# Kernel optimization log

Hardware: AMD Instinct MI355X
Metric: run time of the kernel (lower is better)

## Reference

```python
import math
import jax, jax.numpy as jnp
import numpy as np

N_HEAD = 8
EPS = 1e-4

def _ln(x, g, b):
    m = jnp.mean(x, axis=-1, keepdims=True)
    v = jnp.mean((x - m) ** 2, axis=-1, keepdims=True)
    return (x - m) * jax.lax.rsqrt(v + EPS) * g + b

def _rel_bias(T, rel_w):
    # rel_pos_mat[i,j] = j - i, shifted to [0, 2T-2]; one-hot @ W == table lookup
    pos = jnp.arange(T)
    idx = pos[None, :] - pos[:, None] + (T - 1)        # [T,T]
    return rel_w[idx].transpose(2, 0, 1)               # [n_head,T,T]

def _attn(x, qw, qb, kw, kb, vw, vb, pw, pb, rel_pos):
    B, T, C = x.shape
    hd = C // N_HEAD
    q = (x @ qw + qb).reshape(B, T, N_HEAD, hd)
    k = (x @ kw + kb).reshape(B, T, N_HEAD, hd)
    v = (x @ vw + vb).reshape(B, T, N_HEAD, hd)
    att = jnp.einsum('bqhd,bkhd->bhqk', q, k) * (1.0 / math.sqrt(hd))
    att = att + rel_pos[None]
    att = jax.nn.softmax(att, axis=-1)
    y = jnp.einsum('bhqk,bkhd->bqhd', att, v).reshape(B, T, C)
    return y @ pw + pb

def setup_inputs() -> dict:
    key = jax.random.key(0)
    C, H, W, B = 512, 64, 64, 8
    ks = iter(jax.random.split(key, 40))
    d = {}
    d['x'] = jax.random.normal(next(ks), (B, H * W, C), jnp.float32)
    def w(shape):
        return jax.random.normal(next(ks), shape, jnp.float32) * 0.02
    for p in ('row', 'col'):
        for nm in ('q', 'k', 'v', 'p'):
            d[f'{p}_{nm}w'] = w((C, C))
            d[f'{p}_{nm}b'] = jnp.zeros((C,), jnp.float32)
    for nm in ('rln1', 'cln1', 'ln2'):
        d[f'{nm}_g'] = jnp.ones((C,), jnp.float32)
        d[f'{nm}_b'] = jnp.zeros((C,), jnp.float32)
    d['ff_w1'] = w((C, 4 * C)); d['ff_b1'] = jnp.zeros((4 * C,), jnp.float32)
    d['ff_w2'] = w((4 * C, C)); d['ff_b2'] = jnp.zeros((C,), jnp.float32)
    d['row_rel_w'] = w((2 * H - 1, N_HEAD))
    d['col_rel_w'] = w((2 * W - 1, N_HEAD))
    return d

def reference(x,
              row_qw, row_qb, row_kw, row_kb, row_vw, row_vb, row_pw, row_pb,
              col_qw, col_qb, col_kw, col_kb, col_vw, col_vb, col_pw, col_pb,
              rln1_g, rln1_b, cln1_g, cln1_b, ln2_g, ln2_b,
              ff_w1, ff_b1, ff_w2, ff_b2, row_rel_w, col_rel_w):
    b, n, c = x.shape
    h = w = int(math.isqrt(n))
    # row attention: over h within each column -> batch b*w
    xr = x.reshape(b, h, w, c).transpose(0, 2, 1, 3).reshape(b * w, h, c)
    x_row = _attn(_ln(xr, rln1_g, rln1_b),
                  row_qw, row_qb, row_kw, row_kb, row_vw, row_vb, row_pw, row_pb,
                  _rel_bias(h, row_rel_w))
    x_row = x_row.reshape(b, w, h, c).transpose(0, 2, 1, 3).reshape(b, h * w, c)
    # col attention: over w within each row -> batch b*h
    xc = xr.reshape(b, w, h, c).transpose(0, 2, 1, 3).reshape(b * h, w, c)
    x_col = _attn(_ln(xc, cln1_g, cln1_b),
                  col_qw, col_qb, col_kw, col_kb, col_vw, col_vb, col_pw, col_pb,
                  _rel_bias(w, col_rel_w))
    x_col = x_col.reshape(b, h * w, c)
    out = x + x_row + x_col
    hdd = _ln(out, ln2_g, ln2_b) @ ff_w1 + ff_b1
    hdd = jax.nn.gelu(hdd, approximate=False)
    out = out + (hdd @ ff_w2 + ff_b2)
    return out
```

## Files before the change

kernel.cpp:

```cpp
#include <hip/hip_runtime.h>

typedef unsigned short u16;
typedef unsigned int   u32;
typedef float  f32x4  __attribute__((ext_vector_type(4)));
typedef u32    u32x4  __attribute__((ext_vector_type(4)));
typedef __bf16 bf16x8 __attribute__((ext_vector_type(8)));

#define DEV __device__ __forceinline__

DEV float b2f(u16 u){ return __uint_as_float(((u32)u) << 16); }
DEV u16 f2b(float f){
  u32 u = __float_as_uint(f);
  u32 r = 0x7FFFu + ((u >> 16) & 1u);
  return (u16)((u + r) >> 16);
}
DEV u32 pack2(float a, float b){ return (u32)f2b(a) | ((u32)f2b(b) << 16); }
DEV uint4 pack8(const float* o){
  uint4 r;
  r.x = pack2(o[0], o[1]); r.y = pack2(o[2], o[3]);
  r.z = pack2(o[4], o[5]); r.w = pack2(o[6], o[7]);
  return r;
}

DEV f32x4 mfma16(u32x4 a, u32x4 b, f32x4 c){
  return __builtin_amdgcn_mfma_f32_16x16x32_bf16(
      __builtin_bit_cast(bf16x8, a), __builtin_bit_cast(bf16x8, b), c, 0, 0, 0);
}

DEV void gload16(const u16* g, u16* l){
  __builtin_amdgcn_global_load_lds((const __attribute__((address_space(1))) void*)(g),
                                   (__attribute__((address_space(3))) void*)(l), 16, 0, 0);
}

__global__ __launch_bounds__(256) void tranb3(
    const float* __restrict__ sA, const float* __restrict__ sB,
    const float* __restrict__ sC,
    u16* __restrict__ dA, u16* __restrict__ dB, u16* __restrict__ dC){
  __shared__ float tile[32][33];
  const float* src = (blockIdx.z == 0) ? sA : (blockIdx.z == 1) ? sB : sC;
  u16* dst = (blockIdx.z == 0) ? dA : (blockIdx.z == 1) ? dB : dC;
  const int bx = blockIdx.x * 32, by = blockIdx.y * 32;
  const int tx = threadIdx.x, ty = threadIdx.y;
#pragma unroll
  for (int i = 0; i < 4; ++i)
    tile[ty + i * 8][tx] = src[(size_t)(by + ty + i * 8) * 512 + bx + tx];
  __syncthreads();
#pragma unroll
  for (int i = 0; i < 4; ++i)
    dst[(size_t)(bx + ty + i * 8) * 512 + by + tx] = f2b(tile[tx][ty + i * 8]);
}

__global__ __launch_bounds__(256) void tranbP(const float* __restrict__ src,
                                              u16* __restrict__ dst, int off){
  __shared__ float tile[32][33];
  const int bx = blockIdx.x * 32, by = blockIdx.y * 32;
  const int tx = threadIdx.x, ty = threadIdx.y;
#pragma unroll
  for (int i = 0; i < 4; ++i)
    tile[ty + i * 8][tx] = src[(size_t)(by + ty + i * 8) * 512 + bx + tx];
  __syncthreads();
#pragma unroll
  for (int i = 0; i < 4; ++i)
    dst[(size_t)(bx + ty + i * 8) * 1024 + off + by + tx] = f2b(tile[tx][ty + i * 8]);
}

__global__ __launch_bounds__(256) void tranb(const float* __restrict__ src, u16* __restrict__ dst,
                                             int R, int C){
  __shared__ float tile[32][33];
  const int bx = blockIdx.x * 32, by = blockIdx.y * 32;
  const int tx = threadIdx.x, ty = threadIdx.y;
#pragma unroll
  for (int i = 0; i < 4; ++i)
    tile[ty + i * 8][tx] = src[(size_t)(by + ty + i * 8) * C + bx + tx];
  __syncthreads();
#pragma unroll
  for (int i = 0; i < 4; ++i)
    dst[(size_t)(bx + ty + i * 8) * R + by + tx] = f2b(tile[tx][ty + i * 8]);
}

template<int TWO>
__global__ __launch_bounds__(256) void ln_k(const float* __restrict__ x,
    const float* __restrict__ g1, const float* __restrict__ b1,
    const float* __restrict__ g2, const float* __restrict__ b2,
    u16* __restrict__ y1, u16* __restrict__ y2){
  const int tid = threadIdx.x, lane = tid & 63, wv = tid >> 6;
  const size_t row  = (size_t)blockIdx.x * 4 + wv;
  const size_t boff = row * 512 + lane * 8;
  float f[8];
  {
    const f32x4* p = (const f32x4*)(x + boff);
    const f32x4 a = p[0], b = p[1];
#pragma unroll
    for (int j = 0; j < 4; ++j){ f[j] = a[j]; f[4 + j] = b[j]; }
  }
  float s1 = 0.f, s2 = 0.f;
#pragma unroll
  for (int j = 0; j < 8; ++j){ s1 += f[j]; s2 += f[j] * f[j]; }
#pragma unroll
  for (int off = 32; off > 0; off >>= 1){
    s1 += __shfl_xor(s1, off);
    s2 += __shfl_xor(s2, off);
  }
  const float m   = s1 * (1.0f / 512.0f);
  const float var = s2 * (1.0f / 512.0f) - m * m;
  const float inv = rsqrtf(var + 1e-4f);
  const int cb = lane * 8;
  float o[8];
#pragma unroll
  for (int j = 0; j < 8; ++j) o[j] = (f[j] - m) * inv * g1[cb + j] + b1[cb + j];
  *(uint4*)(y1 + boff) = pack8(o);
  if (TWO){
#pragma unroll
    for (int j = 0; j < 8; ++j) o[j] = (f[j] - m) * inv * g2[cb + j] + b2[cb + j];
    *(uint4*)(y2 + boff) = pack8(o);
  }
}

template<int EPI, bool FUSE3>
__global__ __launch_bounds__(512, 4) void gemmW(const u16* __restrict__ A,
    const u16* __restrict__ A2nd, int nkA,
    const u16* __restrict__ Bt, int ldb,
    const float* __restrict__ b0p, const float* __restrict__ b1p,
    const float* __restrict__ b2p,
    const float* __restrict__ res,
    void* __restrict__ out0, void* __restrict__ out1, void* __restrict__ out2,
    int Nd, int K, int lda){
  __shared__ __align__(16) u16 smem[32768];
  const int tid  = threadIdx.x;
  const int lane = tid & 63;
  const int lr = lane & 15, lg = lane >> 4;
  const int wave = tid >> 6;
  const int wm = (wave >> 2) * 64, wn = (wave & 3) * 64;
  const u32 fd  = blockIdx.y * gridDim.x + blockIdx.x;
  const u32 cpx = (gridDim.x * gridDim.y) >> 3;
  const u32 T   = (fd & 7) * cpx + (fd >> 3);
  const int m0 = (T / gridDim.x) * 128, n0 = (T % gridDim.x) * 256;
  const int nk = K >> 5;

  f32x4 acc[4][4] = {};

  auto stage = [&](int buf, int kt){
    const u16* Ap; int kb;
    if (kt < nkA){ Ap = A;    kb = kt * 32; }
    else         { Ap = A2nd; kb = (kt - nkA) * 32; }
    const int kbB = kt * 32;
    const int ao = buf * 12288, bo = ao + 4096;
    {
      const int r = tid >> 2, gc = (tid & 3) ^ ((r >> 1) & 3);
      gload16(Ap + (size_t)(m0 + r) * lda + kb + gc * 8, smem + ao + tid * 8);
    }
#pragma unroll
    for (int i = 0; i < 2; ++i){
      const int c = i * 512 + tid;
      const int r = c >> 2, gc = (c & 3) ^ ((r >> 1) & 3);
      gload16(Bt + (size_t)(n0 + r) * ldb + kbB + gc * 8, smem + bo + c * 8);
    }
  };

  stage(0, 0);
  int cur = 0;
  for (int kt = 0; kt < nk; ++kt){
    if (kt + 1 < nk){
      stage(cur ^ 1, kt + 1);
      asm volatile("s_waitcnt vmcnt(3)" ::: "memory");
    } else {
      asm volatile("s_waitcnt vmcnt(0)" ::: "memory");
    }
    __builtin_amdgcn_s_barrier();
    __builtin_amdgcn_sched_barrier(0);
    const int ao = cur * 12288, bo = ao + 4096;
    u32x4 af[4], bf[4];
#pragma unroll
    for (int mt = 0; mt < 4; ++mt){
      const int row = wm + mt * 16 + lr;
      const int js = lg ^ ((row >> 1) & 3);
      af[mt] = *(const u32x4*)&smem[ao + row * 32 + js * 8];
    }
#pragma unroll
    for (int nt = 0; nt < 4; ++nt){
      const int row = wn + nt * 16 + lr;
      const int js = lg ^ ((row >> 1) & 3);
      bf[nt] = *(const u32x4*)&smem[bo + row * 32 + js * 8];
    }
    __builtin_amdgcn_s_setprio(1);
#pragma unroll
    for (int mt = 0; mt < 4; ++mt)
#pragma unroll
      for (int nt = 0; nt < 4; ++nt)
        acc[mt][nt] = mfma16(af[mt], bf[nt], acc[mt][nt]);
    __builtin_amdgcn_s_setprio(0);
    asm volatile("" ::: "memory");
    __builtin_amdgcn_sched_barrier(0);
    __builtin_amdgcn_s_barrier();
    cur ^= 1;
  }

  if (EPI == 2){
    float* Cf = (float*)smem;
    float* o = (float*)out0;
#pragma unroll
    for (int h = 0; h < 2; ++h){
      if ((wave >> 2) == h){
#pragma unroll
        for (int mt = 0; mt < 4; ++mt)
#pragma unroll
          for (int nt = 0; nt < 4; ++nt){
            const int col = wn + nt * 16 + lr;
            float bv = b0p ? b0p[n0 + col] : 0.0f;
            if (b1p) bv += b1p[n0 + col];
#pragma unroll
            for (int r = 0; r < 4; ++r)
              Cf[(mt * 16 + lg * 4 + r) * 256 + col] = acc[mt][nt][r] + bv;
          }
      }
      __syncthreads();
#pragma unroll
      for (int p = 0; p < 8; ++p){
        const int rr = p * 8 + (tid >> 6);
        const int cc = (tid & 63) * 4;
        f32x4 c = *(f32x4*)&Cf[rr * 256 + cc];
        const size_t gi = (size_t)(m0 + h * 64 + rr) * Nd + n0 + cc;
        c += *(const f32x4*)(res + gi);
        *(f32x4*)(o + gi) = c;
      }
      __syncthreads();
    }
  } else {
    u16* Cl = smem;
#pragma unroll
    for (int mt = 0; mt < 4; ++mt)
#pragma unroll
      for (int nt = 0; nt < 4; ++nt){
        const int col = n0 + wn + nt * 16 + lr;
        float bv;
        if (FUSE3){
          if (col >= 1024)      bv = b2p[col - 1024];
          else if (col >= 512)  bv = b1p[col - 512];
          else                  bv = b0p[col];
        } else bv = b0p[col];
#pragma unroll
        for (int r = 0; r < 4; ++r){
          float v2 = acc[mt][nt][r] + bv;
          if (EPI == 1) v2 = 0.5f * v2 * (1.0f + erff(v2 * 0.70710678118654752f));
          Cl[(wm + mt * 16 + lg * 4 + r) * 256 + wn + nt * 16 + lr] = f2b(v2);
        }
      }
    __syncthreads();
    u16* o = (u16*)out0;
    int ncol = n0;
    if (FUSE3){
      const int grp = n0 >> 9;
      o = (u16*)(grp == 0 ? out0 : grp == 1 ? out1 : out2);
      ncol = n0 & 511;
    }
#pragma unroll
    for (int p = 0; p < 8; ++p){
      const int rr = p * 16 + (tid >> 5);
      const int cc = (tid & 31) * 8;
      *(uint4*)(o + (size_t)(m0 + rr) * (FUSE3 ? 512 : Nd) + ncol + cc) =
          *(uint4*)&Cl[rr * 256 + cc];
    }
  }
}

__global__ __launch_bounds__(256, 2) void attn64(u16* __restrict__ q,
    const u16* __restrict__ k, const u16* __restrict__ v,
    const float* __restrict__ relw,
    int sscale, int tstr){
  __shared__ __align__(16) u16 Qs[64 * 80];
  __shared__ __align__(16) u16 Ks[64 * 80];
  __shared__ __align__(16) u16 Vt[64 * 80];
  __shared__ __align__(16) u16 Ps[64 * 80];
  __shared__ float Ss[64 * 68];
  __shared__ float tb[128];

  const int s = blockIdx.x, head = blockIdx.y;
  const int tid = threadIdx.x;
  const int lane = tid & 63, wv = tid >> 6;
  const int lr = lane & 15, lg = lane >> 4;
  const int base = (s >> 6) * 4096 + (s & 63) * sscale;

  if (tid < 127) tb[tid] = relw[tid * 8 + head];

#pragma unroll
  for (int rep = 0; rep < 2; ++rep){
    const int e = rep * 2048 + tid * 8;
    const int t = e >> 6, c = e & 63;
    const size_t goff = (size_t)(base + t * tstr) * 512 + head * 64 + c;
    *(uint4*)&Qs[t * 80 + c] = *(const uint4*)(q + goff);
    *(uint4*)&Ks[t * 80 + c] = *(const uint4*)(k + goff);
    const uint4 vvv = *(const uint4*)(v + goff);
    u32 w;
    w = vvv.x; Vt[(c + 0) * 80 + t] = (u16)w; Vt[(c + 1) * 80 + t] = (u16)(w >> 16);
    w = vvv.y; Vt[(c + 2) * 80 + t] = (u16)w; Vt[(c + 3) * 80 + t] = (u16)(w >> 16);
    w = vvv.z; Vt[(c + 4) * 80 + t] = (u16)w; Vt[(c + 5) * 80 + t] = (u16)(w >> 16);
    w = vvv.w; Vt[(c + 6) * 80 + t] = (u16)w; Vt[(c + 7) * 80 + t] = (u16)(w >> 16);
  }
  __syncthreads();

  const int i0 = wv * 16;
  u32x4 af[2];
#pragma unroll
  for (int kk = 0; kk < 2; ++kk)
    af[kk] = *(const u32x4*)&Qs[(i0 + lr) * 80 + kk * 32 + lg * 8];
#pragma unroll
  for (int jt = 0; jt < 4; ++jt){
    f32x4 acc = {};
#pragma unroll
    for (int kk = 0; kk < 2; ++kk){
      const u32x4 bf = *(const u32x4*)&Ks[(jt * 16 + lr) * 80 + kk * 32 + lg * 8];
      acc = mfma16(af[kk], bf, acc);
    }
#pragma unroll
    for (int r = 0; r < 4; ++r){
      const int i = i0 + lg * 4 + r;
      const int j = jt * 16 + lr;
      Ss[i * 68 + j] = acc[r] * 0.125f + tb[j - i + 63];
    }
  }
  __syncthreads();

  {
    const int rr = tid >> 2, cp = tid & 3;
    float ev[16];
    float mx = -3.0e38f;
#pragma unroll
    for (int u = 0; u < 16; ++u){ ev[u] = Ss[rr * 68 + cp * 16 + u]; mx = fmaxf(mx, ev[u]); }
    mx = fmaxf(mx, __shfl_xor(mx, 1, 4));
    mx = fmaxf(mx, __shfl_xor(mx, 2, 4));
    float sum = 0.f;
#pragma unroll
    for (int u = 0; u < 16; ++u){ ev[u] = expf(ev[u] - mx); sum += ev[u]; }
    sum += __shfl_xor(sum, 1, 4);
    sum += __shfl_xor(sum, 2, 4);
    const float inv = 1.0f / sum;
#pragma unroll
    for (int u = 0; u < 16; ++u) Ps[rr * 80 + cp * 16 + u] = f2b(ev[u] * inv);
  }
  __syncthreads();

  u32x4 pa[2];
#pragma unroll
  for (int kk = 0; kk < 2; ++kk)
    pa[kk] = *(const u32x4*)&Ps[(i0 + lr) * 80 + kk * 32 + lg * 8];
#pragma unroll
  for (int dt = 0; dt < 4; ++dt){
    f32x4 acc = {};
#pragma unroll
    for (int kk = 0; kk < 2; ++kk){
      const u32x4 bf = *(const u32x4*)&Vt[(dt * 16 + lr) * 80 + kk * 32 + lg * 8];
      acc = mfma16(pa[kk], bf, acc);
    }
#pragma unroll
    for (int r = 0; r < 4; ++r)
      Qs[(i0 + lg * 4 + r) * 80 + dt * 16 + lr] = f2b(acc[r]);
  }
  __syncthreads();

#pragma unroll
  for (int p = 0; p < 2; ++p){
    const int rr = p * 32 + (tid >> 3);
    const int cc = (tid & 7) * 8;
    *(uint4*)(q + (size_t)(base + rr * tstr) * 512 + head * 64 + cc) =
        *(uint4*)&Qs[rr * 80 + cc];
  }
}

extern "C" void kernel_launch(void* const* d_in, const int* in_sizes, int n_in,
                              void* d_out, int out_size, void* d_ws, size_t ws_size,
                              hipStream_t stream){
  const float* x      = (const float*)d_in[0];
  const float* row_qw = (const float*)d_in[1];  const float* row_qb = (const float*)d_in[2];
  const float* row_kw = (const float*)d_in[3];  const float* row_kb = (const float*)d_in[4];
  const float* row_vw = (const float*)d_in[5];  const float* row_vb = (const float*)d_in[6];
  const float* row_pw = (const float*)d_in[7];  const float* row_pb = (const float*)d_in[8];
  const float* col_qw = (const float*)d_in[9];  const float* col_qb = (const float*)d_in[10];
  const float* col_kw = (const float*)d_in[11]; const float* col_kb = (const float*)d_in[12];
  const float* col_vw = (const float*)d_in[13]; const float* col_vb = (const float*)d_in[14];
  const float* col_pw = (const float*)d_in[15]; const float* col_pb = (const float*)d_in[16];
  const float* rg  = (const float*)d_in[17]; const float* rb  = (const float*)d_in[18];
  const float* cg  = (const float*)d_in[19]; const float* cb  = (const float*)d_in[20];
  const float* l2g = (const float*)d_in[21]; const float* l2b = (const float*)d_in[22];
  const float* ffw1 = (const float*)d_in[23]; const float* ffb1 = (const float*)d_in[24];
  const float* ffw2 = (const float*)d_in[25]; const float* ffb2 = (const float*)d_in[26];
  const float* rrel = (const float*)d_in[27]; const float* crel = (const float*)d_in[28];
  float* outp = (float*)d_out;
  u16* outp16 = (u16*)d_out;

  const size_t ACT = (size_t)32768 * 512;
  const size_t W55 = (size_t)512 * 512;
  const size_t NEED = (4 * ACT + 8 * W55) * 2;
  if (ws_size < NEED) return;

  u16* A0 = (u16*)d_ws;
  u16* A1 = A0 + ACT;
  u16* A2 = A1 + ACT;
  u16* A3 = A2 + ACT;
  u16* D0 = outp16;
  u16* D1 = outp16 + ACT;
  u16* wtb = A3 + ACT;
  u16* wt_q = wtb;  u16* wt_k = wtb + W55;  u16* wt_v = wtb + 2 * W55;
  u16* wt_p = wtb + 3 * W55;
  u16* f1t  = wtb;
  u16* f2t  = wtb + 4 * W55;
  u16* hid  = A1;

  const dim3 tpb(32, 8);
  const dim3 gQKV(6, 256);
  const dim3 gProj(2, 256);
  const dim3 gFF1(4, 256);
  const dim3 gFF2(2, 256);
  const dim3 gAttn(512, 8);

  ln_k<1><<<8192, 256, 0, stream>>>(x, rg, rb, cg, cb, A0, D0);

  tranb3<<<dim3(16, 16, 3), tpb, 0, stream>>>(row_qw, row_kw, row_vw, wt_q, wt_k, wt_v);
  tranbP<<<dim3(16, 16), tpb, 0, stream>>>(row_pw, wt_p, 0);
  gemmW<0, true><<<gQKV, 512, 0, stream>>>(A0, A0, 999, wt_q, 512,
      row_qb, row_kb, row_vb, nullptr, A1, A2, A3, 512, 512, 512);
  attn64<<<gAttn, 256, 0, stream>>>(A1, A2, A3, rrel, 1, 64);

  tranb3<<<dim3(16, 16, 3), tpb, 0, stream>>>(col_qw, col_kw, col_vw, wt_q, wt_k, wt_v);
  tranbP<<<dim3(16, 16), tpb, 0, stream>>>(col_pw, wt_p, 512);
  gemmW<0, true><<<gQKV, 512, 0, stream>>>(D0, D0, 999, wt_q, 512,
      col_qb, col_kb, col_vb, nullptr, A2, A3, D1, 512, 512, 512);
  attn64<<<gAttn, 256, 0, stream>>>(A2, A3, D1, crel, 64, 1);

  gemmW<2, false><<<gProj, 512, 0, stream>>>(A1, A2, 16, wt_p, 1024,
      row_pb, col_pb, nullptr, x, outp, nullptr, nullptr, 512, 1024, 512);

  ln_k<0><<<8192, 256, 0, stream>>>(outp, l2g, l2b, nullptr, nullptr, A0, nullptr);
  tranb<<<dim3(64, 16), tpb, 0, stream>>>(ffw1, f1t, 512, 2048);
  tranb<<<dim3(16, 64), tpb, 0, stream>>>(ffw2, f2t, 2048, 512);
  gemmW<1, false><<<gFF1, 512, 0, stream>>>(A0, A0, 999, f1t, 512,
      ffb1, nullptr, nullptr, nullptr, hid, nullptr, nullptr, 1024, 512, 512);
  gemmW<2, false><<<gFF2, 512, 0, stream>>>(hid, hid, 999, f2t, 2048,
      ffb2, nullptr, nullptr, outp, outp, nullptr, nullptr, 512, 1024, 1024);
  gemmW<1, false><<<gFF1, 512, 0, stream>>>(A0, A0, 999, f1t + (size_t)1024 * 512, 512,
      ffb1 + 1024, nullptr, nullptr, nullptr, hid, nullptr, nullptr, 1024, 512, 512);
  gemmW<2, false><<<gFF2, 512, 0, stream>>>(hid, hid, 999, f2t + 1024, 2048,
      nullptr, nullptr, nullptr, outp, outp, nullptr, nullptr, 512, 1024, 1024);
}
```

Before: 499.1 us.

## Enlarge GEMM tiles to 256x256 with triple-buffered split A/B staging

The GEMM kernel now computes a 256x256 output tile per block instead of 128x256. Each wave holds 8x4 accumulators, and the grid is halved in M. Global-to-LDS staging moves to a three-stage ring with separate A and B loads, interleaved between two MFMA half-steps, so operand reuse goes up and more load latency is hidden. In exchange, register and LDS use roughly double, occupancy drops to 2 blocks per CU, and there are fewer blocks (768 for QKV, 256 for proj/FF2) to fill the CUs.

```diff
diff --git a/kernel.cpp b/kernel.cpp
--- a/kernel.cpp
+++ b/kernel.cpp
@@ -117,7 +117,7 @@
 }
 
 template<int EPI, bool FUSE3>
-__global__ __launch_bounds__(512, 4) void gemmW(const u16* __restrict__ A,
+__global__ __launch_bounds__(512, 2) void gemm256(const u16* __restrict__ A,
     const u16* __restrict__ A2nd, int nkA,
     const u16* __restrict__ Bt, int ldb,
     const float* __restrict__ b0p, const float* __restrict__ b1p,
@@ -125,63 +125,64 @@
     const float* __restrict__ res,
     void* __restrict__ out0, void* __restrict__ out1, void* __restrict__ out2,
     int Nd, int K, int lda){
-  __shared__ __align__(16) u16 smem[32768];
+  __shared__ __align__(16) u16 smem[65536];
   const int tid  = threadIdx.x;
   const int lane = tid & 63;
   const int lr = lane & 15, lg = lane >> 4;
   const int wave = tid >> 6;
-  const int wm = (wave >> 2) * 64, wn = (wave & 3) * 64;
+  const int wm = (wave >> 2) * 128, wn = (wave & 3) * 64;
   const u32 fd  = blockIdx.y * gridDim.x + blockIdx.x;
   const u32 cpx = (gridDim.x * gridDim.y) >> 3;
   const u32 T   = (fd & 7) * cpx + (fd >> 3);
-  const int m0 = (T / gridDim.x) * 128, n0 = (T % gridDim.x) * 256;
+  const int m0 = (T / gridDim.x) * 256, n0 = (T % gridDim.x) * 256;
   const int nk = K >> 5;
 
-  f32x4 acc[4][4] = {};
-
-  auto stage = [&](int buf, int kt){
+  f32x4 acc[8][4] = {};
+
+  auto stageA = [&](int t){
     const u16* Ap; int kb;
-    if (kt < nkA){ Ap = A;    kb = kt * 32; }
-    else         { Ap = A2nd; kb = (kt - nkA) * 32; }
-    const int kbB = kt * 32;
-    const int ao = buf * 12288, bo = ao + 4096;
-    {
-      const int r = tid >> 2, gc = (tid & 3) ^ ((r >> 1) & 3);
-      gload16(Ap + (size_t)(m0 + r) * lda + kb + gc * 8, smem + ao + tid * 8);
-    }
+    if (t < nkA){ Ap = A;    kb = t * 32; }
+    else        { Ap = A2nd; kb = (t - nkA) * 32; }
+    const int so = (t % 3) * 16384;
 #pragma unroll
     for (int i = 0; i < 2; ++i){
       const int c = i * 512 + tid;
       const int r = c >> 2, gc = (c & 3) ^ ((r >> 1) & 3);
-      gload16(Bt + (size_t)(n0 + r) * ldb + kbB + gc * 8, smem + bo + c * 8);
+      gload16(Ap + (size_t)(m0 + r) * lda + kb + gc * 8, smem + so + c * 8);
     }
   };
-
-  stage(0, 0);
-  int cur = 0;
-  for (int kt = 0; kt < nk; ++kt){
-    if (kt + 1 < nk){
-      stage(cur ^ 1, kt + 1);
-      asm volatile("s_waitcnt vmcnt(3)" ::: "memory");
-    } else {
-      asm volatile("s_waitcnt vmcnt(0)" ::: "memory");
-    }
-    __builtin_amdgcn_s_barrier();
-    __builtin_amdgcn_sched_barrier(0);
-    const int ao = cur * 12288, bo = ao + 4096;
+  auto stageB = [&](int t){
+    const int so = (t % 3) * 16384 + 8192;
+    const int kb = t * 32;
+#pragma unroll
+    for (int i = 0; i < 2; ++i){
+      const int c = i * 512 + tid;
+      const int r = c >> 2, gc = (c & 3) ^ ((r >> 1) & 3);
+      gload16(Bt + (size_t)(n0 + r) * ldb + kb + gc * 8, smem + so + c * 8);
+    }
+  };
+
+  stageB(0); stageA(0); stageB(1); stageA(1);
+  asm volatile("s_waitcnt vmcnt(4)" ::: "memory");
+  __builtin_amdgcn_s_barrier();
+
+  for (int t = 0; t < nk; ++t){
+    const int so = (t % 3) * 16384;
     u32x4 af[4], bf[4];
+#pragma unroll
+    for (int nt = 0; nt < 4; ++nt){
+      const int row = wn + nt * 16 + lr;
+      bf[nt] = *(const u32x4*)&smem[so + 8192 + row * 32 + ((lg ^ ((row >> 1) & 3)) << 3)];
+    }
 #pragma unroll
     for (int mt = 0; mt < 4; ++mt){
       const int row = wm + mt * 16 + lr;
-      const int js = lg ^ ((row >> 1) & 3);
-      af[mt] = *(const u32x4*)&smem[ao + row * 32 + js * 8];
-    }
-#pragma unroll
-    for (int nt = 0; nt < 4; ++nt){
-      const int row = wn + nt * 16 + lr;
-      const int js = lg ^ ((row >> 1) & 3);
-      bf[nt] = *(const u32x4*)&smem[bo + row * 32 + js * 8];
-    }
+      af[mt] = *(const u32x4*)&smem[so + row * 32 + ((lg ^ ((row >> 1) & 3)) << 3)];
+    }
+    if (t + 2 < nk) stageB(t + 2);
+    __builtin_amdgcn_s_barrier();
+    asm volatile("s_waitcnt lgkmcnt(0)" ::: "memory");
+    __builtin_amdgcn_sched_barrier(0);
     __builtin_amdgcn_s_setprio(1);
 #pragma unroll
     for (int mt = 0; mt < 4; ++mt)
@@ -189,11 +190,31 @@
       for (int nt = 0; nt < 4; ++nt)
         acc[mt][nt] = mfma16(af[mt], bf[nt], acc[mt][nt]);
     __builtin_amdgcn_s_setprio(0);
-    asm volatile("" ::: "memory");
     __builtin_amdgcn_sched_barrier(0);
+#pragma unroll
+    for (int mt = 0; mt < 4; ++mt){
+      const int row = wm + 64 + mt * 16 + lr;
+      af[mt] = *(const u32x4*)&smem[so + row * 32 + ((lg ^ ((row >> 1) & 3)) << 3)];
+    }
+    if (t + 2 < nk){
+      stageA(t + 2);
+      asm volatile("s_waitcnt vmcnt(4)" ::: "memory");
+    } else if (t + 1 < nk){
+      asm volatile("s_waitcnt vmcnt(0)" ::: "memory");
+    }
     __builtin_amdgcn_s_barrier();
-    cur ^= 1;
-  }
+    asm volatile("s_waitcnt lgkmcnt(0)" ::: "memory");
+    __builtin_amdgcn_sched_barrier(0);
+    __builtin_amdgcn_s_setprio(1);
+#pragma unroll
+    for (int mt = 0; mt < 4; ++mt)
+#pragma unroll
+      for (int nt = 0; nt < 4; ++nt)
+        acc[4 + mt][nt] = mfma16(af[mt], bf[nt], acc[4 + mt][nt]);
+    __builtin_amdgcn_s_setprio(0);
+    __builtin_amdgcn_sched_barrier(0);
+  }
+  __syncthreads();
 
   if (EPI == 2){
     float* Cf = (float*)smem;
@@ -202,7 +223,7 @@
     for (int h = 0; h < 2; ++h){
       if ((wave >> 2) == h){
 #pragma unroll
-        for (int mt = 0; mt < 4; ++mt)
+        for (int m = 0; m < 8; ++m)
 #pragma unroll
           for (int nt = 0; nt < 4; ++nt){
             const int col = wn + nt * 16 + lr;
@@ -210,16 +231,16 @@
             if (b1p) bv += b1p[n0 + col];
 #pragma unroll
             for (int r = 0; r < 4; ++r)
-              Cf[(mt * 16 + lg * 4 + r) * 256 + col] = acc[mt][nt][r] + bv;
+              Cf[(m * 16 + lg * 4 + r) * 256 + col] = acc[m][nt][r] + bv;
           }
       }
       __syncthreads();
 #pragma unroll
-      for (int p = 0; p < 8; ++p){
+      for (int p = 0; p < 16; ++p){
         const int rr = p * 8 + (tid >> 6);
         const int cc = (tid & 63) * 4;
         f32x4 c = *(f32x4*)&Cf[rr * 256 + cc];
-        const size_t gi = (size_t)(m0 + h * 64 + rr) * Nd + n0 + cc;
+        const size_t gi = (size_t)(m0 + h * 128 + rr) * Nd + n0 + cc;
         c += *(const f32x4*)(res + gi);
         *(f32x4*)(o + gi) = c;
       }
@@ -228,7 +249,7 @@
   } else {
     u16* Cl = smem;
 #pragma unroll
-    for (int mt = 0; mt < 4; ++mt)
+    for (int m = 0; m < 8; ++m)
 #pragma unroll
       for (int nt = 0; nt < 4; ++nt){
         const int col = n0 + wn + nt * 16 + lr;
@@ -240,9 +261,9 @@
         } else bv = b0p[col];
 #pragma unroll
         for (int r = 0; r < 4; ++r){
-          float v2 = acc[mt][nt][r] + bv;
+          float v2 = acc[m][nt][r] + bv;
           if (EPI == 1) v2 = 0.5f * v2 * (1.0f + erff(v2 * 0.70710678118654752f));
-          Cl[(wm + mt * 16 + lg * 4 + r) * 256 + wn + nt * 16 + lr] = f2b(v2);
+          Cl[(wm + m * 16 + lg * 4 + r) * 256 + wn + nt * 16 + lr] = f2b(v2);
         }
       }
     __syncthreads();
@@ -254,7 +275,7 @@
       ncol = n0 & 511;
     }
 #pragma unroll
-    for (int p = 0; p < 8; ++p){
+    for (int p = 0; p < 16; ++p){
       const int rr = p * 16 + (tid >> 5);
       const int cc = (tid & 31) * 8;
       *(uint4*)(o + (size_t)(m0 + rr) * (FUSE3 ? 512 : Nd) + ncol + cc) =
@@ -406,38 +427,38 @@
   u16* hid  = A1;
 
   const dim3 tpb(32, 8);
-  const dim3 gQKV(6, 256);
-  const dim3 gProj(2, 256);
-  const dim3 gFF1(4, 256);
-  const dim3 gFF2(2, 256);
+  const dim3 gQKV(6, 128);
+  const dim3 gProj(2, 128);
+  const dim3 gFF1(4, 128);
+  const dim3 gFF2(2, 128);
   const dim3 gAttn(512, 8);
 
   ln_k<1><<<8192, 256, 0, stream>>>(x, rg, rb, cg, cb, A0, D0);
 
   tranb3<<<dim3(16, 16, 3), tpb, 0, stream>>>(row_qw, row_kw, row_vw, wt_q, wt_k, wt_v);
   tranbP<<<dim3(16, 16), tpb, 0, stream>>>(row_pw, wt_p, 0);
-  gemmW<0, true><<<gQKV, 512, 0, stream>>>(A0, A0, 999, wt_q, 512,
+  gemm256<0, true><<<gQKV, 512, 0, stream>>>(A0, A0, 999, wt_q, 512,
       row_qb, row_kb, row_vb, nullptr, A1, A2, A3, 512, 512, 512);
   attn64<<<gAttn, 256, 0, stream>>>(A1, A2, A3, rrel, 1, 64);
 
   tranb3<<<dim3(16, 16, 3), tpb, 0, stream>>>(col_qw, col_kw, col_vw, wt_q, wt_k, wt_v);
   tranbP<<<dim3(16, 16), tpb, 0, stream>>>(col_pw, wt_p, 512);
-  gemmW<0, true><<<gQKV, 512, 0, stream>>>(D0, D0, 999, wt_q, 512,
+  gemm256<0, true><<<gQKV, 512, 0, stream>>>(D0, D0, 999, wt_q, 512,
       col_qb, col_kb, col_vb, nullptr, A2, A3, D1, 512, 512, 512);
   attn64<<<gAttn, 256, 0, stream>>>(A2, A3, D1, crel, 64, 1);
 
-  gemmW<2, false><<<gProj, 512, 0, stream>>>(A1, A2, 16, wt_p, 1024,
+  gemm256<2, false><<<gProj, 512, 0, stream>>>(A1, A2, 16, wt_p, 1024,
       row_pb, col_pb, nullptr, x, outp, nullptr, nullptr, 512, 1024, 512);
 
   ln_k<0><<<8192, 256, 0, stream>>>(outp, l2g, l2b, nullptr, nullptr, A0, nullptr);
   tranb<<<dim3(64, 16), tpb, 0, stream>>>(ffw1, f1t, 512, 2048);
   tranb<<<dim3(16, 64), tpb, 0, stream>>>(ffw2, f2t, 2048, 512);
-  gemmW<1, false><<<gFF1, 512, 0, stream>>>(A0, A0, 999, f1t, 512,
+  gemm256<1, false><<<gFF1, 512, 0, stream>>>(A0, A0, 999, f1t, 512,
       ffb1, nullptr, nullptr, nullptr, hid, nullptr, nullptr, 1024, 512, 512);
-  gemmW<2, false><<<gFF2, 512, 0, stream>>>(hid, hid, 999, f2t, 2048,
+  gemm256<2, false><<<gFF2, 512, 0, stream>>>(hid, hid, 999, f2t, 2048,
       ffb2, nullptr, nullptr, outp, outp, nullptr, nullptr, 512, 1024, 1024);
-  gemmW<1, false><<<gFF1, 512, 0, stream>>>(A0, A0, 999, f1t + (size_t)1024 * 512, 512,
+  gemm256<1, false><<<gFF1, 512, 0, stream>>>(A0, A0, 999, f1t + (size_t)1024 * 512, 512,
       ffb1 + 1024, nullptr, nullptr, nullptr, hid, nullptr, nullptr, 1024, 512, 512);
-  gemmW<2, false><<<gFF2, 512, 0, stream>>>(hid, hid, 999, f2t + 1024, 2048,
+  gemm256<2, false><<<gFF2, 512, 0, stream>>>(hid, hid, 999, f2t + 1024, 2048,
       nullptr, nullptr, nullptr, outp, outp, nullptr, nullptr, 512, 1024, 1024);
 }
```

After: 639.7 us. 28.2% more time.
